# Kernel tuning notes

Measured on AMD Instinct MI355X. Metric: run time of the kernel, lower is better.

Reference implementation:

```python
import jax, jax.numpy as jnp
import numpy as np

D = 256; H = 8; FF = 1024; Q = 128; C = 512; B = 4
HD = D // H

def _ln(x, g, b):
    m = x.mean(-1, keepdims=True)
    v = ((x - m) ** 2).mean(-1, keepdims=True)
    return (x - m) / jnp.sqrt(v + 1e-5) * g + b

def _mha(q, k, v, in_w, in_b, out_w, out_b):
    # q,k,v: (L,B,D) / (S,B,D); in_w: (3D,D) packed q|k|v as in torch MHA
    qp = q @ in_w[:D].T + in_b[:D]
    kp = k @ in_w[D:2*D].T + in_b[D:2*D]
    vp = v @ in_w[2*D:].T + in_b[2*D:]
    L, Bb, _ = qp.shape; S = kp.shape[0]
    qh = qp.reshape(L, Bb, H, HD)
    kh = kp.reshape(S, Bb, H, HD)
    vh = vp.reshape(S, Bb, H, HD)
    scores = jnp.einsum('lbhd,sbhd->bhls', qh, kh) / np.sqrt(HD).astype(np.float32)
    a = jax.nn.softmax(scores, axis=-1)
    o = jnp.einsum('bhls,sbhd->lbhd', a, vh).reshape(L, Bb, D)
    return o @ out_w.T + out_b

def setup_inputs() -> dict:
    key = jax.random.key(0)
    ks = jax.random.split(key, 30)
    def p(k, shape, s=0.02):
        return jax.random.normal(k, shape, jnp.float32) * s
    return {
        'tgt': jax.random.normal(ks[0], (Q, B, D), jnp.float32),
        'memory': jax.random.normal(ks[1], (C, B, D), jnp.float32),
        'query_pos': jax.random.normal(ks[2], (Q, B, D), jnp.float32),
        'relative_pos': jax.random.normal(ks[3], (Q, C, B, D), jnp.float32),
        'ln1_g': jnp.ones((D,), jnp.float32), 'ln1_b': jnp.zeros((D,), jnp.float32),
        'ln2_g': jnp.ones((D,), jnp.float32), 'ln2_b': jnp.zeros((D,), jnp.float32),
        'ln3_g': jnp.ones((D,), jnp.float32), 'ln3_b': jnp.zeros((D,), jnp.float32),
        'in_proj_w': p(ks[4], (3 * D, D)), 'in_proj_b': jnp.zeros((3 * D,), jnp.float32),
        'attn_out_w': p(ks[5], (D, D)), 'attn_out_b': jnp.zeros((D,), jnp.float32),
        'mlp1_w': p(ks[6], (D, D)), 'mlp1_b': jnp.zeros((D,), jnp.float32),
        'mlp2_w': p(ks[7], (D, D)), 'mlp2_b': jnp.zeros((D,), jnp.float32),
        'v_w': p(ks[8], (D, D)), 'v_b': jnp.zeros((D,), jnp.float32),
        'o_w': p(ks[9], (D, D)), 'o_b': jnp.zeros((D,), jnp.float32),
        'ff1_w': p(ks[10], (FF, D)), 'ff1_b': jnp.zeros((FF,), jnp.float32),
        'ff2_w': p(ks[11], (D, FF)), 'ff2_b': jnp.zeros((D,), jnp.float32),
    }

def reference(tgt, memory, query_pos, relative_pos,
              ln1_g, ln1_b, ln2_g, ln2_b, ln3_g, ln3_b,
              in_proj_w, in_proj_b, attn_out_w, attn_out_b,
              mlp1_w, mlp1_b, mlp2_w, mlp2_b,
              v_w, v_b, o_w, o_b, ff1_w, ff1_b, ff2_w, ff2_b):
    # pre-norm self-attention (dropout = identity in eval)
    tgt2 = _ln(tgt, ln1_g, ln1_b)
    qk = tgt2 + query_pos
    sa = _mha(qk, qk, tgt2, in_proj_w, in_proj_b, attn_out_w, attn_out_b)
    tgt = tgt + sa
    # relation-attention branch
    tgt2 = _ln(tgt, ln2_g, ln2_b)                       # (Q,B,D)
    x = tgt2[:, None, :, :] - memory[None, :, :, :] + relative_pos  # (Q,C,B,D)
    h = jax.nn.relu(x @ mlp1_w.T + mlp1_b)
    sim = h @ mlp2_w.T + mlp2_b                          # (Q,C,B,D)
    attn = jax.nn.softmax(sim / np.sqrt(D).astype(np.float32), axis=1)
    v2 = (memory[None, :, :, :] + relative_pos) @ v_w.T + v_b
    t = jnp.einsum('qcbf,qcbf->qbf', attn, v2)           # (Q,B,D)
    t = jax.nn.relu(t @ o_w.T + o_b)
    tgt = t + tgt2
    # FFN
    tgt2 = _ln(tgt, ln3_g, ln3_b)
    ff = jax.nn.relu(tgt2 @ ff1_w.T + ff1_b) @ ff2_w.T + ff2_b
    return tgt + ff
```

## Files before the change

kernel.cpp:

```cpp
#include <hip/hip_runtime.h>
#include <hip/hip_bf16.h>
#include <cstdint>
#include <cstddef>

#define DEV __device__ __forceinline__

typedef __attribute__((ext_vector_type(8))) short short8;
typedef __attribute__((ext_vector_type(4))) float f32x4;

constexpr int Dm  = 256;
constexpr int Qn  = 128;
constexpr int Cn  = 512;
constexpr int Bn  = 4;

DEV unsigned short f2bf(float f){
  unsigned int u = __builtin_bit_cast(unsigned int, f);
  u += 0x7fffu + ((u >> 16) & 1u);
  return (unsigned short)(u >> 16);
}
DEV unsigned int pk2(float a, float b){
  return (unsigned int)f2bf(a) | ((unsigned int)f2bf(b) << 16);
}

DEV f32x4 mfma16(short8 a, short8 b, f32x4 c){
  return __builtin_amdgcn_mfma_f32_16x16x32_bf16(a, b, c, 0, 0, 0);
}

DEV short8 ldfrag(const unsigned short* buf, int rowbytes, int row0, int ks, int l){
  int r = row0 + (l & 15);
  int byte = (ks * 64 + ((l >> 4) * 16)) ^ ((r & 7) << 4);
  return *(const short8*)((const char*)buf + r * rowbytes + byte);
}

DEV void gload_lds16(const void* g, void* lds){
  __builtin_amdgcn_global_load_lds(
      (const __attribute__((address_space(1))) unsigned int*)g,
      (__attribute__((address_space(3))) unsigned int*)lds, 16, 0, 0);
}

DEV void packw(unsigned short* dst, const float* src, int j){
  int f = j >> 8, d = j & 255;
  int d8 = d >> 3, e = d & 7;
  int byte = (d8 * 16) ^ ((f & 15) << 4);
  dst[f * 256 + (byte >> 1) + e] = f2bf(src[j]);
}

__global__ __launch_bounds__(256) void conv_all_kernel(
    const float* inw, unsigned short* inw_bf,
    const float* aow, unsigned short* aow_bf,
    const float* ow,  unsigned short* ow_bf,
    const float* f1w, unsigned short* f1w_bf,
    const float* f2w, unsigned short* f2w_bf,
    const float* m1w, unsigned short* w1pk,
    const float* m2w, unsigned short* w2pk,
    const float* vw,  unsigned short* wvpk)
{
  const int total = 196608 + 65536 + 65536 + 262144 + 262144 + 3 * 65536;
  for (int i = blockIdx.x * 256 + threadIdx.x; i < total; i += gridDim.x * 256){
    int j = i;
    if (j < 196608){ inw_bf[j] = f2bf(inw[j]); continue; } j -= 196608;
    if (j < 65536) { aow_bf[j] = f2bf(aow[j]); continue; } j -= 65536;
    if (j < 65536) { ow_bf[j]  = f2bf(ow[j]);  continue; } j -= 65536;
    if (j < 262144){ f1w_bf[j] = f2bf(f1w[j]); continue; } j -= 262144;
    if (j < 262144){ f2w_bf[j] = f2bf(f2w[j]); continue; } j -= 262144;
    if (j < 65536) { packw(w1pk, m1w, j); continue; } j -= 65536;
    if (j < 65536) { packw(w2pk, m2w, j); continue; } j -= 65536;
    packw(wvpk, vw, j);
  }
}

__global__ __launch_bounds__(256) void ln_kernel(
    const float* __restrict__ in, const float* __restrict__ g, const float* __restrict__ bt,
    const float* __restrict__ addp,
    float* __restrict__ outF, unsigned short* __restrict__ outA, unsigned short* __restrict__ outB)
{
  const int r = blockIdx.x, t = threadIdx.x;
  float x = in[(size_t)r * 256 + t];
  float s = x, s2 = x * x;
  #pragma unroll
  for (int m = 1; m < 64; m <<= 1){ s += __shfl_xor(s, m, 64); s2 += __shfl_xor(s2, m, 64); }
  __shared__ float ls[8];
  int w = t >> 6, l = t & 63;
  if (l == 0){ ls[w] = s; ls[4 + w] = s2; }
  __syncthreads();
  s  = ls[0] + ls[1] + ls[2] + ls[3];
  s2 = ls[4] + ls[5] + ls[6] + ls[7];
  float mean = s * (1.f / 256.f);
  float var  = s2 * (1.f / 256.f) - mean * mean;
  float y = (x - mean) * rsqrtf(var + 1e-5f) * g[t] + bt[t];
  size_t o = (size_t)r * 256 + t;
  if (outF) outF[o] = y;
  if (outA) outA[o] = f2bf(y);
  if (outB) outB[o] = f2bf(y + addp[o]);
}

__global__ __launch_bounds__(256, 4) void gemm_kernel(
    const unsigned short* __restrict__ A, const unsigned short* __restrict__ W,
    const float* __restrict__ bias, const float* __restrict__ resid,
    float* __restrict__ Cf, unsigned short* __restrict__ Cb,
    int M, int N, int K, float alpha, int relu)
{
  __shared__ unsigned short As[64 * 64];
  __shared__ unsigned short Ws[64 * 64];
  const int tid = threadIdx.x;
  const int l = tid & 63;
  const int w = tid >> 6;
  const int wm = w >> 1, wn = w & 1;
  const int bm = blockIdx.x * 64, bn = blockIdx.y * 64;
  f32x4 acc[2][2] = {{{0,0,0,0},{0,0,0,0}},{{0,0,0,0},{0,0,0,0}}};

  for (int kc = 0; kc < K; kc += 64){
    __syncthreads();
    #pragma unroll
    for (int i = 0; i < 2; ++i){
      int idx = tid + i * 256;
      int r = idx >> 3, s = idx & 7;
      int byte = (s * 16) ^ ((r & 7) << 4);
      *(short8*)((char*)As + r * 128 + byte) = *(const short8*)(A + (size_t)(bm + r) * K + kc + s * 8);
      *(short8*)((char*)Ws + r * 128 + byte) = *(const short8*)(W + (size_t)(bn + r) * K + kc + s * 8);
    }
    __syncthreads();
    #pragma unroll
    for (int ks = 0; ks < 2; ++ks){
      short8 af[2], bf[2];
      af[0] = ldfrag(As, 128, wm * 32,      ks, l);
      af[1] = ldfrag(As, 128, wm * 32 + 16, ks, l);
      bf[0] = ldfrag(Ws, 128, wn * 32,      ks, l);
      bf[1] = ldfrag(Ws, 128, wn * 32 + 16, ks, l);
      #pragma unroll
      for (int i = 0; i < 2; ++i)
        #pragma unroll
        for (int j = 0; j < 2; ++j)
          acc[i][j] = mfma16(af[i], bf[j], acc[i][j]);
    }
  }
  #pragma unroll
  for (int i = 0; i < 2; ++i)
  #pragma unroll
  for (int j = 0; j < 2; ++j){
    int col = bn + wn * 32 + j * 16 + (l & 15);
    float bv = bias ? bias[col] : 0.f;
    #pragma unroll
    for (int u = 0; u < 4; ++u){
      int row = bm + wm * 32 + i * 16 + ((l >> 4) << 2) + u;
      float v = alpha * acc[i][j][u] + bv;
      if (relu) v = fmaxf(v, 0.f);
      if (resid) v += resid[(size_t)row * N + col];
      if (Cf) Cf[(size_t)row * N + col] = v;
      if (Cb) Cb[(size_t)row * N + col] = f2bf(v);
    }
  }
}

__global__ __launch_bounds__(256) void attn_kernel(
    const float* __restrict__ qkp, const float* __restrict__ vp,
    unsigned short* __restrict__ attn_o)
{
  __shared__ float ks[128][33];
  __shared__ float vs[128][33];
  __shared__ float sc[128][129];
  const int bh = blockIdx.x;
  const int b = bh >> 3, h = bh & 7;
  const int tid = threadIdx.x;
  const int lrow = tid >> 1;
  const int half = tid & 1;
  {
    int s = tid >> 1;
    int d0 = half * 16;
    const float* kp = qkp + ((size_t)s * Bn + b) * 512 + 256 + h * 32 + d0;
    const float* vv = vp  + ((size_t)s * Bn + b) * 256 +       h * 32 + d0;
    #pragma unroll
    for (int d = 0; d < 16; d += 4){
      *(float4*)&ks[s][d0 + d] = *(const float4*)(kp + d);
      *(float4*)&vs[s][d0 + d] = *(const float4*)(vv + d);
    }
  }
  __syncthreads();
  float qv[32];
  const float* qp = qkp + ((size_t)lrow * Bn + b) * 512 + h * 32;
  #pragma unroll
  for (int d = 0; d < 32; ++d) qv[d] = qp[d];
  const float scale = 0.17677669529663687f;
  float mloc = -1e30f;
  for (int s2 = 0; s2 < 64; ++s2){
    int s = half * 64 + s2;
    float dot = 0.f;
    #pragma unroll
    for (int d = 0; d < 32; ++d) dot += qv[d] * ks[s][d];
    dot *= scale;
    sc[lrow][s] = dot;
    mloc = fmaxf(mloc, dot);
  }
  float m = fmaxf(mloc, __shfl_xor(mloc, 1, 64));
  float sum = 0.f;
  for (int s2 = 0; s2 < 64; ++s2){
    int s = half * 64 + s2;
    float e = __expf(sc[lrow][s] - m);
    sum += e;
    sc[lrow][s] = e;
  }
  sum += __shfl_xor(sum, 1, 64);
  float inv = 1.f / sum;
  float o[32];
  #pragma unroll
  for (int d = 0; d < 32; ++d) o[d] = 0.f;
  for (int s2 = 0; s2 < 64; ++s2){
    int s = half * 64 + s2;
    float e = sc[lrow][s];
    #pragma unroll
    for (int d = 0; d < 32; ++d) o[d] += e * vs[s][d];
  }
  #pragma unroll
  for (int d = 0; d < 32; ++d){
    o[d] += __shfl_xor(o[d], 1, 64);
    o[d] *= inv;
  }
  unsigned short* op = attn_o + ((size_t)lrow * Bn + b) * 256 + h * 32 + half * 16;
  #pragma unroll
  for (int d = 0; d < 16; ++d) op[d] = f2bf(o[half * 16 + d]);
}

__global__ __launch_bounds__(512, 2) void relfused_kernel(
    const float* __restrict__ rel, const float* __restrict__ memp,
    const float* __restrict__ t22f,
    const unsigned short* __restrict__ W1g,
    const unsigned short* __restrict__ W2g,
    const unsigned short* __restrict__ Wvg,
    const float* __restrict__ b1, const float* __restrict__ b2,
    const float* __restrict__ vbp,
    unsigned short* __restrict__ trel)
{
  __shared__ unsigned short W1t[65536];
  __shared__ unsigned short xb[4096];
  __shared__ unsigned short yb[4096];
  __shared__ unsigned short hb[4096];

  const int qb = blockIdx.x;
  const int q = qb >> 2, b = qb & 3;
  const int tid = threadIdx.x;
  const int w = tid >> 6, l = tid & 63;
  const int l15 = l & 15, lg = l >> 4;

  #pragma unroll
  for (int i = 0; i < 16; ++i){
    int base = (w * 16 + i) * 64;
    gload_lds16((const char*)W1g + ((size_t)base + l) * 16, (char*)W1t + (size_t)base * 16);
  }

  short8 w2r[2][8], wvr[2][8];
  #pragma unroll
  for (int j = 0; j < 2; ++j){
    int f = w * 32 + j * 16 + l15;
    #pragma unroll
    for (int kc = 0; kc < 8; ++kc){
      int byte = f * 512 + ((kc * 64 + lg * 16) ^ ((f & 15) << 4));
      w2r[j][kc] = *(const short8*)((const char*)W2g + byte);
      wvr[j][kc] = *(const short8*)((const char*)Wvg + byte);
    }
  }

  float bv1[2][4], bv2[2][4], bvv[2][4];
  #pragma unroll
  for (int j = 0; j < 2; ++j)
    #pragma unroll
    for (int u = 0; u < 4; ++u){
      int f = w * 32 + j * 16 + lg * 4 + u;
      bv1[j][u] = b1[f]; bv2[j][u] = b2[f]; bvv[j][u] = vbp[f];
    }

  const int srow = tid >> 5, d8 = tid & 31;
  const int toff = srow * 512 + ((d8 * 16) ^ ((srow & 15) << 4));
  const float4 t20 = *(const float4*)(t22f + (size_t)qb * 256 + d8 * 8);
  const float4 t21 = *(const float4*)(t22f + (size_t)qb * 256 + d8 * 8 + 4);
  const float* relbase = rel + (((size_t)q * 512 + srow) * 4 + b) * 256 + d8 * 8;
  const float* membase = memp + ((size_t)(srow * 4 + b)) * 256 + d8 * 8;

  float4 r0 = *(const float4*)relbase;
  float4 r1 = *(const float4*)(relbase + 4);
  float4 m0 = *(const float4*)membase;
  float4 m1 = *(const float4*)(membase + 4);

  float ta[2][4], la[2][4];
  #pragma unroll
  for (int j = 0; j < 2; ++j)
    #pragma unroll
    for (int u = 0; u < 4; ++u){ ta[j][u] = 0.f; la[j][u] = 0.f; }

  for (int t = 0; t < 32; ++t){
    uint4 xw, yw;
    xw.x = pk2(t20.x - m0.x + r0.x, t20.y - m0.y + r0.y);
    xw.y = pk2(t20.z - m0.z + r0.z, t20.w - m0.w + r0.w);
    xw.z = pk2(t21.x - m1.x + r1.x, t21.y - m1.y + r1.y);
    xw.w = pk2(t21.z - m1.z + r1.z, t21.w - m1.w + r1.w);
    yw.x = pk2(r0.x + m0.x, r0.y + m0.y);
    yw.y = pk2(r0.z + m0.z, r0.w + m0.w);
    yw.z = pk2(r1.x + m1.x, r1.y + m1.y);
    yw.w = pk2(r1.z + m1.z, r1.w + m1.w);
    *(uint4*)((char*)xb + toff) = xw;
    *(uint4*)((char*)yb + toff) = yw;
    if (t < 31){
      const float* rp = relbase + (size_t)(t + 1) * 16384;
      const float* mp = membase + (size_t)(t + 1) * 16384;
      r0 = *(const float4*)rp;  r1 = *(const float4*)(rp + 4);
      m0 = *(const float4*)mp;  m1 = *(const float4*)(mp + 4);
    }
    if (t == 0) asm volatile("s_waitcnt vmcnt(0)" ::: "memory");
    __syncthreads();

    f32x4 acch[2] = {{0,0,0,0},{0,0,0,0}};
    #pragma unroll
    for (int kc = 0; kc < 8; ++kc){
      short8 bx = *(const short8*)((const char*)xb + l15 * 512 + ((kc * 64 + lg * 16) ^ (l15 << 4)));
      #pragma unroll
      for (int j = 0; j < 2; ++j){
        int f = w * 32 + j * 16 + l15;
        short8 aw = *(const short8*)((const char*)W1t + f * 512 + ((kc * 64 + lg * 16) ^ ((f & 15) << 4)));
        acch[j] = mfma16(aw, bx, acch[j]);
      }
    }
    #pragma unroll
    for (int j = 0; j < 2; ++j){
      uint2 hp;
      hp.x = pk2(fmaxf(acch[j][0] + bv1[j][0], 0.f), fmaxf(acch[j][1] + bv1[j][1], 0.f));
      hp.y = pk2(fmaxf(acch[j][2] + bv1[j][2], 0.f), fmaxf(acch[j][3] + bv1[j][3], 0.f));
      int inrow = (w * 64 + j * 32 + lg * 8) ^ (l15 << 4);
      *(uint2*)((char*)hb + l15 * 512 + inrow) = hp;
    }
    __syncthreads();

    f32x4 accs[2] = {{0,0,0,0},{0,0,0,0}};
    f32x4 accv[2] = {{0,0,0,0},{0,0,0,0}};
    #pragma unroll
    for (int kc = 0; kc < 8; ++kc){
      int inb = (kc * 64 + lg * 16) ^ (l15 << 4);
      short8 bh = *(const short8*)((const char*)hb + l15 * 512 + inb);
      short8 by = *(const short8*)((const char*)yb + l15 * 512 + inb);
      #pragma unroll
      for (int j = 0; j < 2; ++j){
        accs[j] = mfma16(w2r[j][kc], bh, accs[j]);
        accv[j] = mfma16(wvr[j][kc], by, accv[j]);
      }
    }
    #pragma unroll
    for (int j = 0; j < 2; ++j)
      #pragma unroll
      for (int u = 0; u < 4; ++u){
        float e = __expf((accs[j][u] + bv2[j][u]) * 0.0625f);
        float v2 = accv[j][u] + bvv[j][u];
        ta[j][u] += e * v2;
        la[j][u] += e;
      }
    if (t < 31) __syncthreads();
  }

  #pragma unroll
  for (int j = 0; j < 2; ++j)
    #pragma unroll
    for (int u = 0; u < 4; ++u){
      #pragma unroll
      for (int m = 1; m <= 8; m <<= 1){
        ta[j][u] += __shfl_xor(ta[j][u], m, 64);
        la[j][u] += __shfl_xor(la[j][u], m, 64);
      }
    }
  if (l15 == 0){
    #pragma unroll
    for (int j = 0; j < 2; ++j){
      uint2 o;
      o.x = pk2(ta[j][0] / la[j][0], ta[j][1] / la[j][1]);
      o.y = pk2(ta[j][2] / la[j][2], ta[j][3] / la[j][3]);
      *(uint2*)(trel + (size_t)qb * 256 + w * 32 + j * 16 + lg * 4) = o;
    }
  }
}

extern "C" void kernel_launch(void* const* d_in, const int* in_sizes, int n_in,
                              void* d_out, int out_size, void* d_ws, size_t ws_size,
                              hipStream_t stream)
{
  const float* tgt  = (const float*)d_in[0];
  const float* mem  = (const float*)d_in[1];
  const float* qpos = (const float*)d_in[2];
  const float* rel  = (const float*)d_in[3];
  const float* ln1g = (const float*)d_in[4];
  const float* ln1b = (const float*)d_in[5];
  const float* ln2g = (const float*)d_in[6];
  const float* ln2b = (const float*)d_in[7];
  const float* ln3g = (const float*)d_in[8];
  const float* ln3b = (const float*)d_in[9];
  const float* inw  = (const float*)d_in[10];
  const float* inb  = (const float*)d_in[11];
  const float* aow  = (const float*)d_in[12];
  const float* aob  = (const float*)d_in[13];
  const float* m1w  = (const float*)d_in[14];
  const float* m1b  = (const float*)d_in[15];
  const float* m2w  = (const float*)d_in[16];
  const float* m2b  = (const float*)d_in[17];
  const float* vw   = (const float*)d_in[18];
  const float* vb   = (const float*)d_in[19];
  const float* ow   = (const float*)d_in[20];
  const float* ob   = (const float*)d_in[21];
  const float* f1w  = (const float*)d_in[22];
  const float* f1b  = (const float*)d_in[23];
  const float* f2w  = (const float*)d_in[24];
  const float* f2b  = (const float*)d_in[25];

  char* ws = (char*)d_ws;
  size_t off = 0;
  auto alloc = [&](size_t bytes) -> char* {
    char* p = ws + off; off += (bytes + 255) & ~size_t(255); return p;
  };
  unsigned short* w1pk    = (unsigned short*)alloc(256 * 256 * 2);
  unsigned short* w2pk    = (unsigned short*)alloc(256 * 256 * 2);
  unsigned short* wvpk    = (unsigned short*)alloc(256 * 256 * 2);
  unsigned short* inw_bf  = (unsigned short*)alloc(768 * 256 * 2);
  unsigned short* aow_bf  = (unsigned short*)alloc(256 * 256 * 2);
  unsigned short* ow_bf   = (unsigned short*)alloc(256 * 256 * 2);
  unsigned short* f1w_bf  = (unsigned short*)alloc(1024 * 256 * 2);
  unsigned short* f2w_bf  = (unsigned short*)alloc(256 * 1024 * 2);
  unsigned short* t21_bf  = (unsigned short*)alloc(512 * 256 * 2);
  unsigned short* qk_bf   = (unsigned short*)alloc(512 * 256 * 2);
  float*          qkp     = (float*)alloc(512 * 512 * 4);
  float*          vp      = (float*)alloc(512 * 256 * 4);
  unsigned short* ao_bf   = (unsigned short*)alloc(512 * 256 * 2);
  float*          tgta    = (float*)alloc(512 * 256 * 4);
  float*          t22_f   = (float*)alloc(512 * 256 * 4);
  unsigned short* trel_bf = (unsigned short*)alloc(512 * 256 * 2);
  float*          tgtr    = (float*)alloc(512 * 256 * 4);
  unsigned short* t23_bf  = (unsigned short*)alloc(512 * 256 * 2);
  unsigned short* ffh_bf  = (unsigned short*)alloc(512 * 1024 * 2);

  conv_all_kernel<<<2048, 256, 0, stream>>>(inw, inw_bf, aow, aow_bf, ow, ow_bf,
      f1w, f1w_bf, f2w, f2w_bf, m1w, w1pk, m2w, w2pk, vw, wvpk);

  ln_kernel<<<512, 256, 0, stream>>>(tgt, ln1g, ln1b, qpos, nullptr, t21_bf, qk_bf);

  gemm_kernel<<<dim3(8, 8), 256, 0, stream>>>(qk_bf, inw_bf, inb, nullptr,
      qkp, nullptr, 512, 512, 256, 1.f, 0);
  gemm_kernel<<<dim3(8, 4), 256, 0, stream>>>(t21_bf, inw_bf + 512 * 256, inb + 512, nullptr,
      vp, nullptr, 512, 256, 256, 1.f, 0);

  attn_kernel<<<32, 256, 0, stream>>>(qkp, vp, ao_bf);

  gemm_kernel<<<dim3(8, 4), 256, 0, stream>>>(ao_bf, aow_bf, aob, tgt,
      tgta, nullptr, 512, 256, 256, 1.f, 0);

  ln_kernel<<<512, 256, 0, stream>>>(tgta, ln2g, ln2b, nullptr, t22_f, nullptr, nullptr);

  relfused_kernel<<<512, 512, 0, stream>>>(rel, mem, t22_f, w1pk, w2pk, wvpk,
      m1b, m2b, vb, trel_bf);

  gemm_kernel<<<dim3(8, 4), 256, 0, stream>>>(trel_bf, ow_bf, ob, t22_f,
      tgtr, nullptr, 512, 256, 256, 1.f, 1);

  ln_kernel<<<512, 256, 0, stream>>>(tgtr, ln3g, ln3b, nullptr, nullptr, t23_bf, nullptr);

  gemm_kernel<<<dim3(8, 16), 256, 0, stream>>>(t23_bf, f1w_bf, f1b, nullptr,
      nullptr, ffh_bf, 512, 1024, 256, 1.f, 1);
  gemm_kernel<<<dim3(8, 4), 256, 0, stream>>>(ffh_bf, f2w_bf, f2b, tgtr,
      (float*)d_out, nullptr, 512, 256, 1024, 1.f, 0);
}
```

Baseline: 331.0 us.

## Keep W1 in registers, double-buffer relation tiles, fold biases out of loop

The relation kernel now holds W1 in registers instead of a 128KB LDS copy, and double-buffers the x/y/h tiles so the second GEMM stage of step t-1 overlaps with the first stage of step t. The mlp2 bias is dropped, since a per-feature constant cancels in a softmax over C. The v bias is added once after normalisation instead of on every element. This cuts LDS footprint and synchronisation per step, but about 192 registers of weights per thread under launch_bounds(512,2) risks register spilling.

```diff
diff --git a/kernel.cpp b/kernel.cpp
--- a/kernel.cpp
+++ b/kernel.cpp
@@ -30,12 +30,6 @@
   int r = row0 + (l & 15);
   int byte = (ks * 64 + ((l >> 4) * 16)) ^ ((r & 7) << 4);
   return *(const short8*)((const char*)buf + r * rowbytes + byte);
-}
-
-DEV void gload_lds16(const void* g, void* lds){
-  __builtin_amdgcn_global_load_lds(
-      (const __attribute__((address_space(1))) unsigned int*)g,
-      (__attribute__((address_space(3))) unsigned int*)lds, 16, 0, 0);
 }
 
 DEV void packw(unsigned short* dst, const float* src, int j){
@@ -226,14 +220,15 @@
     const unsigned short* __restrict__ W1g,
     const unsigned short* __restrict__ W2g,
     const unsigned short* __restrict__ Wvg,
-    const float* __restrict__ b1, const float* __restrict__ b2,
+    const float* __restrict__ b1,
     const float* __restrict__ vbp,
     unsigned short* __restrict__ trel)
 {
-  __shared__ unsigned short W1t[65536];
-  __shared__ unsigned short xb[4096];
-  __shared__ unsigned short yb[4096];
-  __shared__ unsigned short hb[4096];
+  __shared__ unsigned short xb[2][4096];
+  __shared__ unsigned short yb[2][4096];
+  __shared__ unsigned short hb[2][4096];
+  __shared__ float t2s[256];
+  __shared__ float b1s[256];
 
   const int qb = blockIdx.x;
   const int q = qb >> 2, b = qb & 3;
@@ -241,53 +236,36 @@
   const int w = tid >> 6, l = tid & 63;
   const int l15 = l & 15, lg = l >> 4;
 
-  #pragma unroll
-  for (int i = 0; i < 16; ++i){
-    int base = (w * 16 + i) * 64;
-    gload_lds16((const char*)W1g + ((size_t)base + l) * 16, (char*)W1t + (size_t)base * 16);
-  }
-
-  short8 w2r[2][8], wvr[2][8];
+  if (tid < 256){ t2s[tid] = t22f[(size_t)qb * 256 + tid]; b1s[tid] = b1[tid]; }
+
+  short8 w1r[2][8], w2r[2][8], wvr[2][8];
   #pragma unroll
   for (int j = 0; j < 2; ++j){
     int f = w * 32 + j * 16 + l15;
     #pragma unroll
     for (int kc = 0; kc < 8; ++kc){
       int byte = f * 512 + ((kc * 64 + lg * 16) ^ ((f & 15) << 4));
+      w1r[j][kc] = *(const short8*)((const char*)W1g + byte);
       w2r[j][kc] = *(const short8*)((const char*)W2g + byte);
       wvr[j][kc] = *(const short8*)((const char*)Wvg + byte);
     }
   }
 
-  float bv1[2][4], bv2[2][4], bvv[2][4];
-  #pragma unroll
-  for (int j = 0; j < 2; ++j)
-    #pragma unroll
-    for (int u = 0; u < 4; ++u){
-      int f = w * 32 + j * 16 + lg * 4 + u;
-      bv1[j][u] = b1[f]; bv2[j][u] = b2[f]; bvv[j][u] = vbp[f];
-    }
-
   const int srow = tid >> 5, d8 = tid & 31;
   const int toff = srow * 512 + ((d8 * 16) ^ ((srow & 15) << 4));
-  const float4 t20 = *(const float4*)(t22f + (size_t)qb * 256 + d8 * 8);
-  const float4 t21 = *(const float4*)(t22f + (size_t)qb * 256 + d8 * 8 + 4);
   const float* relbase = rel + (((size_t)q * 512 + srow) * 4 + b) * 256 + d8 * 8;
   const float* membase = memp + ((size_t)(srow * 4 + b)) * 256 + d8 * 8;
 
-  float4 r0 = *(const float4*)relbase;
-  float4 r1 = *(const float4*)(relbase + 4);
-  float4 m0 = *(const float4*)membase;
-  float4 m1 = *(const float4*)(membase + 4);
-
   float ta[2][4], la[2][4];
   #pragma unroll
   for (int j = 0; j < 2; ++j)
     #pragma unroll
     for (int u = 0; u < 4; ++u){ ta[j][u] = 0.f; la[j][u] = 0.f; }
 
-  for (int t = 0; t < 32; ++t){
-    uint4 xw, yw;
+  uint4 xw, yw;
+  auto packxy = [&](const float4& r0, const float4& r1, const float4& m0, const float4& m1){
+    float4 t20 = *(const float4*)&t2s[d8 * 8];
+    float4 t21 = *(const float4*)&t2s[d8 * 8 + 4];
     xw.x = pk2(t20.x - m0.x + r0.x, t20.y - m0.y + r0.y);
     xw.y = pk2(t20.z - m0.z + r0.z, t20.w - m0.w + r0.w);
     xw.z = pk2(t21.x - m1.x + r1.x, t21.y - m1.y + r1.y);
@@ -296,45 +274,18 @@
     yw.y = pk2(r0.z + m0.z, r0.w + m0.w);
     yw.z = pk2(r1.x + m1.x, r1.y + m1.y);
     yw.w = pk2(r1.z + m1.z, r1.w + m1.w);
-    *(uint4*)((char*)xb + toff) = xw;
-    *(uint4*)((char*)yb + toff) = yw;
-    if (t < 31){
-      const float* rp = relbase + (size_t)(t + 1) * 16384;
-      const float* mp = membase + (size_t)(t + 1) * 16384;
-      r0 = *(const float4*)rp;  r1 = *(const float4*)(rp + 4);
-      m0 = *(const float4*)mp;  m1 = *(const float4*)(mp + 4);
-    }
-    if (t == 0) asm volatile("s_waitcnt vmcnt(0)" ::: "memory");
-    __syncthreads();
-
-    f32x4 acch[2] = {{0,0,0,0},{0,0,0,0}};
-    #pragma unroll
-    for (int kc = 0; kc < 8; ++kc){
-      short8 bx = *(const short8*)((const char*)xb + l15 * 512 + ((kc * 64 + lg * 16) ^ (l15 << 4)));
-      #pragma unroll
-      for (int j = 0; j < 2; ++j){
-        int f = w * 32 + j * 16 + l15;
-        short8 aw = *(const short8*)((const char*)W1t + f * 512 + ((kc * 64 + lg * 16) ^ ((f & 15) << 4)));
-        acch[j] = mfma16(aw, bx, acch[j]);
-      }
-    }
-    #pragma unroll
-    for (int j = 0; j < 2; ++j){
-      uint2 hp;
-      hp.x = pk2(fmaxf(acch[j][0] + bv1[j][0], 0.f), fmaxf(acch[j][1] + bv1[j][1], 0.f));
-      hp.y = pk2(fmaxf(acch[j][2] + bv1[j][2], 0.f), fmaxf(acch[j][3] + bv1[j][3], 0.f));
-      int inrow = (w * 64 + j * 32 + lg * 8) ^ (l15 << 4);
-      *(uint2*)((char*)hb + l15 * 512 + inrow) = hp;
-    }
-    __syncthreads();
-
+  };
+
+  auto phase2 = [&](int pb){
+    const char* hbp = (const char*)hb + pb * 8192;
+    const char* ybp = (const char*)yb + pb * 8192;
     f32x4 accs[2] = {{0,0,0,0},{0,0,0,0}};
     f32x4 accv[2] = {{0,0,0,0},{0,0,0,0}};
     #pragma unroll
     for (int kc = 0; kc < 8; ++kc){
-      int inb = (kc * 64 + lg * 16) ^ (l15 << 4);
-      short8 bh = *(const short8*)((const char*)hb + l15 * 512 + inb);
-      short8 by = *(const short8*)((const char*)yb + l15 * 512 + inb);
+      int inb = l15 * 512 + ((kc * 64 + lg * 16) ^ (l15 << 4));
+      short8 bh = *(const short8*)(hbp + inb);
+      short8 by = *(const short8*)(ybp + inb);
       #pragma unroll
       for (int j = 0; j < 2; ++j){
         accs[j] = mfma16(w2r[j][kc], bh, accs[j]);
@@ -345,13 +296,67 @@
     for (int j = 0; j < 2; ++j)
       #pragma unroll
       for (int u = 0; u < 4; ++u){
-        float e = __expf((accs[j][u] + bv2[j][u]) * 0.0625f);
-        float v2 = accv[j][u] + bvv[j][u];
-        ta[j][u] += e * v2;
+        float e = __expf(accs[j][u] * 0.0625f);
+        ta[j][u] += e * accv[j][u];
         la[j][u] += e;
       }
-    if (t < 31) __syncthreads();
-  }
+  };
+
+  float4 r0 = *(const float4*)relbase;
+  float4 r1 = *(const float4*)(relbase + 4);
+  float4 m0 = *(const float4*)membase;
+  float4 m1 = *(const float4*)(membase + 4);
+  __syncthreads();
+  packxy(r0, r1, m0, m1);
+  *(uint4*)((char*)xb + toff) = xw;
+  *(uint4*)((char*)yb + toff) = yw;
+  r0 = *(const float4*)(relbase + 16384);
+  r1 = *(const float4*)(relbase + 16384 + 4);
+  m0 = *(const float4*)(membase + 16384);
+  m1 = *(const float4*)(membase + 16384 + 4);
+
+  for (int t = 0; t < 32; ++t){
+    __syncthreads();
+    const char* xbp = (const char*)xb + (t & 1) * 8192;
+    f32x4 acch[2] = {{0,0,0,0},{0,0,0,0}};
+    #pragma unroll
+    for (int kc = 0; kc < 8; ++kc){
+      short8 bx = *(const short8*)(xbp + l15 * 512 + ((kc * 64 + lg * 16) ^ (l15 << 4)));
+      #pragma unroll
+      for (int j = 0; j < 2; ++j)
+        acch[j] = mfma16(w1r[j][kc], bx, acch[j]);
+    }
+    {
+      char* hbp = (char*)hb + (t & 1) * 8192;
+      #pragma unroll
+      for (int j = 0; j < 2; ++j){
+        float4 bb = *(const float4*)&b1s[w * 32 + j * 16 + lg * 4];
+        uint2 hp;
+        hp.x = pk2(fmaxf(acch[j][0] + bb.x, 0.f), fmaxf(acch[j][1] + bb.y, 0.f));
+        hp.y = pk2(fmaxf(acch[j][2] + bb.z, 0.f), fmaxf(acch[j][3] + bb.w, 0.f));
+        int inrow = (w * 64 + j * 32 + lg * 8) ^ (l15 << 4);
+        *(uint2*)(hbp + l15 * 512 + inrow) = hp;
+      }
+    }
+    if (t < 31) packxy(r0, r1, m0, m1);
+    if (t > 0) phase2((t - 1) & 1);
+    if (t < 31){
+      __syncthreads();
+      char* xbn = (char*)xb + ((t + 1) & 1) * 8192;
+      char* ybn = (char*)yb + ((t + 1) & 1) * 8192;
+      *(uint4*)(xbn + toff) = xw;
+      *(uint4*)(ybn + toff) = yw;
+      if (t < 30){
+        size_t o = (size_t)(t + 2) * 16384;
+        r0 = *(const float4*)(relbase + o);
+        r1 = *(const float4*)(relbase + o + 4);
+        m0 = *(const float4*)(membase + o);
+        m1 = *(const float4*)(membase + o + 4);
+      }
+    }
+  }
+  __syncthreads();
+  phase2(1);
 
   #pragma unroll
   for (int j = 0; j < 2; ++j)
@@ -366,9 +371,10 @@
   if (l15 == 0){
     #pragma unroll
     for (int j = 0; j < 2; ++j){
+      float4 vb4 = *(const float4*)(vbp + w * 32 + j * 16 + lg * 4);
       uint2 o;
-      o.x = pk2(ta[j][0] / la[j][0], ta[j][1] / la[j][1]);
-      o.y = pk2(ta[j][2] / la[j][2], ta[j][3] / la[j][3]);
+      o.x = pk2(ta[j][0] / la[j][0] + vb4.x, ta[j][1] / la[j][1] + vb4.y);
+      o.y = pk2(ta[j][2] / la[j][2] + vb4.z, ta[j][3] / la[j][3] + vb4.w);
       *(uint2*)(trel + (size_t)qb * 256 + w * 32 + j * 16 + lg * 4) = o;
     }
   }
@@ -448,7 +454,7 @@
   ln_kernel<<<512, 256, 0, stream>>>(tgta, ln2g, ln2b, nullptr, t22_f, nullptr, nullptr);
 
   relfused_kernel<<<512, 512, 0, stream>>>(rel, mem, t22_f, w1pk, w2pk, wvpk,
-      m1b, m2b, vb, trel_bf);
+      m1b, vb, trel_bf);
 
   gemm_kernel<<<dim3(8, 4), 256, 0, stream>>>(trel_bf, ow_bf, ob, t22_f,
       tgtr, nullptr, 512, 256, 256, 1.f, 1);
```

New measurement: 373.3 us. 1.13x slower.

## Restructure relation kernel with async double-buffered LDS loads and register weights

Applied to the files above, without the earlier changes.

The relation-attention kernel moves to 1024 threads per block. Each wave now keeps its 16-feature slice of all three weight matrices (W1, W2, Wv) in registers, so W1 no longer has to be staged in LDS. Tiles of relative_pos and a bf16 copy of memory are streamed into double-buffered LDS with global_load_lds, processing 32 context rows per step so the next tile's load overlaps compute. The mlp2 bias is dropped because it is constant along the softmax axis, and the value bias is added after normalisation. Memory is converted to bf16 once in the setup kernel, which adds extra work there and a small rounding change to memory.

```diff
diff --git a/kernel.cpp b/kernel.cpp
--- a/kernel.cpp
+++ b/kernel.cpp
@@ -18,6 +18,8 @@
   u += 0x7fffu + ((u >> 16) & 1u);
   return (unsigned short)(u >> 16);
 }
+DEV float bfl(unsigned int u){ return __builtin_bit_cast(float, u << 16); }
+DEV float bfh(unsigned int u){ return __builtin_bit_cast(float, u & 0xffff0000u); }
 DEV unsigned int pk2(float a, float b){
   return (unsigned int)f2bf(a) | ((unsigned int)f2bf(b) << 16);
 }
@@ -53,9 +55,10 @@
     const float* f2w, unsigned short* f2w_bf,
     const float* m1w, unsigned short* w1pk,
     const float* m2w, unsigned short* w2pk,
-    const float* vw,  unsigned short* wvpk)
-{
-  const int total = 196608 + 65536 + 65536 + 262144 + 262144 + 3 * 65536;
+    const float* vw,  unsigned short* wvpk,
+    const float* memp, unsigned short* mem_bf)
+{
+  const int total = 196608 + 65536 + 65536 + 262144 + 262144 + 3 * 65536 + 524288;
   for (int i = blockIdx.x * 256 + threadIdx.x; i < total; i += gridDim.x * 256){
     int j = i;
     if (j < 196608){ inw_bf[j] = f2bf(inw[j]); continue; } j -= 196608;
@@ -65,7 +68,8 @@
     if (j < 262144){ f2w_bf[j] = f2bf(f2w[j]); continue; } j -= 262144;
     if (j < 65536) { packw(w1pk, m1w, j); continue; } j -= 65536;
     if (j < 65536) { packw(w2pk, m2w, j); continue; } j -= 65536;
-    packw(wvpk, vw, j);
+    if (j < 65536) { packw(wvpk, vw, j);  continue; } j -= 65536;
+    mem_bf[j] = f2bf(memp[j]);
   }
 }
 
@@ -220,20 +224,23 @@
   for (int d = 0; d < 16; ++d) op[d] = f2bf(o[half * 16 + d]);
 }
 
-__global__ __launch_bounds__(512, 2) void relfused_kernel(
-    const float* __restrict__ rel, const float* __restrict__ memp,
+__global__ __launch_bounds__(1024) void relfused_kernel(
+    const float* __restrict__ rel, const unsigned short* __restrict__ mem_bf,
     const float* __restrict__ t22f,
     const unsigned short* __restrict__ W1g,
     const unsigned short* __restrict__ W2g,
     const unsigned short* __restrict__ Wvg,
-    const float* __restrict__ b1, const float* __restrict__ b2,
+    const float* __restrict__ b1,
     const float* __restrict__ vbp,
     unsigned short* __restrict__ trel)
 {
-  __shared__ unsigned short W1t[65536];
-  __shared__ unsigned short xb[4096];
-  __shared__ unsigned short yb[4096];
-  __shared__ unsigned short hb[4096];
+  __shared__ char relbuf[2 * 32768];
+  __shared__ char membuf[2 * 16384];
+  __shared__ char xb[16384];
+  __shared__ char yb[16384];
+  __shared__ char hb[16384];
+  __shared__ float t2s[256];
+  __shared__ float b1s[256];
 
   const int qb = blockIdx.x;
   const int q = qb >> 2, b = qb & 3;
@@ -241,136 +248,134 @@
   const int w = tid >> 6, l = tid & 63;
   const int l15 = l & 15, lg = l >> 4;
 
-  #pragma unroll
-  for (int i = 0; i < 16; ++i){
-    int base = (w * 16 + i) * 64;
-    gload_lds16((const char*)W1g + ((size_t)base + l) * 16, (char*)W1t + (size_t)base * 16);
-  }
-
-  short8 w2r[2][8], wvr[2][8];
-  #pragma unroll
-  for (int j = 0; j < 2; ++j){
-    int f = w * 32 + j * 16 + l15;
+  if (tid < 256){ t2s[tid] = t22f[(size_t)qb * 256 + tid]; b1s[tid] = b1[tid]; }
+
+  short8 w1r[8], w2r[8], wvr[8];
+  {
+    const size_t F = (size_t)(w * 16 + l15);
     #pragma unroll
     for (int kc = 0; kc < 8; ++kc){
-      int byte = f * 512 + ((kc * 64 + lg * 16) ^ ((f & 15) << 4));
-      w2r[j][kc] = *(const short8*)((const char*)W2g + byte);
-      wvr[j][kc] = *(const short8*)((const char*)Wvg + byte);
-    }
-  }
-
-  float bv1[2][4], bv2[2][4], bvv[2][4];
-  #pragma unroll
-  for (int j = 0; j < 2; ++j)
-    #pragma unroll
-    for (int u = 0; u < 4; ++u){
-      int f = w * 32 + j * 16 + lg * 4 + u;
-      bv1[j][u] = b1[f]; bv2[j][u] = b2[f]; bvv[j][u] = vbp[f];
-    }
-
-  const int srow = tid >> 5, d8 = tid & 31;
-  const int toff = srow * 512 + ((d8 * 16) ^ ((srow & 15) << 4));
-  const float4 t20 = *(const float4*)(t22f + (size_t)qb * 256 + d8 * 8);
-  const float4 t21 = *(const float4*)(t22f + (size_t)qb * 256 + d8 * 8 + 4);
-  const float* relbase = rel + (((size_t)q * 512 + srow) * 4 + b) * 256 + d8 * 8;
-  const float* membase = memp + ((size_t)(srow * 4 + b)) * 256 + d8 * 8;
-
-  float4 r0 = *(const float4*)relbase;
-  float4 r1 = *(const float4*)(relbase + 4);
-  float4 m0 = *(const float4*)membase;
-  float4 m1 = *(const float4*)(membase + 4);
-
-  float ta[2][4], la[2][4];
-  #pragma unroll
-  for (int j = 0; j < 2; ++j)
-    #pragma unroll
-    for (int u = 0; u < 4; ++u){ ta[j][u] = 0.f; la[j][u] = 0.f; }
-
-  for (int t = 0; t < 32; ++t){
-    uint4 xw, yw;
-    xw.x = pk2(t20.x - m0.x + r0.x, t20.y - m0.y + r0.y);
-    xw.y = pk2(t20.z - m0.z + r0.z, t20.w - m0.w + r0.w);
-    xw.z = pk2(t21.x - m1.x + r1.x, t21.y - m1.y + r1.y);
-    xw.w = pk2(t21.z - m1.z + r1.z, t21.w - m1.w + r1.w);
-    yw.x = pk2(r0.x + m0.x, r0.y + m0.y);
-    yw.y = pk2(r0.z + m0.z, r0.w + m0.w);
-    yw.z = pk2(r1.x + m1.x, r1.y + m1.y);
-    yw.w = pk2(r1.z + m1.z, r1.w + m1.w);
-    *(uint4*)((char*)xb + toff) = xw;
-    *(uint4*)((char*)yb + toff) = yw;
-    if (t < 31){
-      const float* rp = relbase + (size_t)(t + 1) * 16384;
-      const float* mp = membase + (size_t)(t + 1) * 16384;
-      r0 = *(const float4*)rp;  r1 = *(const float4*)(rp + 4);
-      m0 = *(const float4*)mp;  m1 = *(const float4*)(mp + 4);
-    }
-    if (t == 0) asm volatile("s_waitcnt vmcnt(0)" ::: "memory");
+      size_t byte = F * 512 + (size_t)((kc * 64 + lg * 16) ^ (l15 << 4));
+      w1r[kc] = *(const short8*)((const char*)W1g + byte);
+      w2r[kc] = *(const short8*)((const char*)W2g + byte);
+      wvr[kc] = *(const short8*)((const char*)Wvg + byte);
+    }
+  }
+
+  auto issue = [&](int tp){
+    const int p = tp & 1;
+    const int c0 = tp * 32;
+    #pragma unroll
+    for (int i = 0; i < 2; ++i){
+      int c = c0 + 2 * w + i;
+      gload_lds16(rel + (((size_t)q * 512 + c) * 4 + b) * 256 + l * 4,
+                  relbuf + p * 32768 + (2 * w + i) * 1024);
+    }
+    int c = c0 + 2 * w + (l >> 5);
+    gload_lds16(mem_bf + ((size_t)(c * 4 + b)) * 256 + (l & 31) * 8,
+                membuf + p * 16384 + w * 1024);
+  };
+
+  float ta[4] = {0.f, 0.f, 0.f, 0.f}, la[4] = {0.f, 0.f, 0.f, 0.f};
+
+  issue(0);
+
+  for (int t = 0; t < 16; ++t){
+    if (t < 15){
+      issue(t + 1);
+      asm volatile("s_waitcnt vmcnt(3)" ::: "memory");
+    } else {
+      asm volatile("s_waitcnt vmcnt(0)" ::: "memory");
+    }
+    __builtin_amdgcn_sched_barrier(0);
     __syncthreads();
 
-    f32x4 acch[2] = {{0,0,0,0},{0,0,0,0}};
-    #pragma unroll
-    for (int kc = 0; kc < 8; ++kc){
-      short8 bx = *(const short8*)((const char*)xb + l15 * 512 + ((kc * 64 + lg * 16) ^ (l15 << 4)));
+    {
+      const int cr = tid >> 5, d8 = tid & 31;
+      const char* rbp = relbuf + (t & 1) * 32768 + cr * 1024;
+      const char* mbp = membuf + (t & 1) * 16384 + cr * 512;
+      int swz = (cr & 15) << 4;
+      int bo1 = cr * 512 + ((((d8 >> 1) * 16) ^ swz) | ((d8 & 1) * 8));
+      int bo2 = cr * 512 + ((((16 + (d8 >> 1)) * 16) ^ swz) | ((d8 & 1) * 8));
+      {
+        float4 ra = *(const float4*)(rbp + d8 * 16);
+        uint2  ma = *(const uint2*)(mbp + d8 * 8);
+        float4 t4 = *(const float4*)((const char*)t2s + d8 * 16);
+        float m0 = bfl(ma.x), m1 = bfh(ma.x), m2 = bfl(ma.y), m3 = bfh(ma.y);
+        uint2 xw, yw;
+        xw.x = pk2(t4.x - m0 + ra.x, t4.y - m1 + ra.y);
+        xw.y = pk2(t4.z - m2 + ra.z, t4.w - m3 + ra.w);
+        yw.x = pk2(ra.x + m0, ra.y + m1);
+        yw.y = pk2(ra.z + m2, ra.w + m3);
+        *(uint2*)(xb + bo1) = xw;
+        *(uint2*)(yb + bo1) = yw;
+      }
+      {
+        float4 ra = *(const float4*)(rbp + 512 + d8 * 16);
+        uint2  ma = *(const uint2*)(mbp + 256 + d8 * 8);
+        float4 t4 = *(const float4*)((const char*)t2s + 512 + d8 * 16);
+        float m0 = bfl(ma.x), m1 = bfh(ma.x), m2 = bfl(ma.y), m3 = bfh(ma.y);
+        uint2 xw, yw;
+        xw.x = pk2(t4.x - m0 + ra.x, t4.y - m1 + ra.y);
+        xw.y = pk2(t4.z - m2 + ra.z, t4.w - m3 + ra.w);
+        yw.x = pk2(ra.x + m0, ra.y + m1);
+        yw.y = pk2(ra.z + m2, ra.w + m3);
+        *(uint2*)(xb + bo2) = xw;
+        *(uint2*)(yb + bo2) = yw;
+      }
+    }
+    __syncthreads();
+
+    #pragma unroll
+    for (int cs = 0; cs < 2; ++cs){
+      f32x4 acc = {0.f, 0.f, 0.f, 0.f};
+      const char* xrow = xb + (cs * 16 + l15) * 512;
       #pragma unroll
-      for (int j = 0; j < 2; ++j){
-        int f = w * 32 + j * 16 + l15;
-        short8 aw = *(const short8*)((const char*)W1t + f * 512 + ((kc * 64 + lg * 16) ^ ((f & 15) << 4)));
-        acch[j] = mfma16(aw, bx, acch[j]);
+      for (int kc = 0; kc < 8; ++kc)
+        acc = mfma16(w1r[kc], *(const short8*)(xrow + ((kc * 64 + lg * 16) ^ (l15 << 4))), acc);
+      float4 bb = *(const float4*)&b1s[w * 16 + lg * 4];
+      uint2 hp;
+      hp.x = pk2(fmaxf(acc[0] + bb.x, 0.f), fmaxf(acc[1] + bb.y, 0.f));
+      hp.y = pk2(fmaxf(acc[2] + bb.z, 0.f), fmaxf(acc[3] + bb.w, 0.f));
+      int ro = w * 32 + lg * 8;
+      *(uint2*)(hb + (cs * 16 + l15) * 512 + (((ro & ~15) ^ (l15 << 4)) | (ro & 8))) = hp;
+    }
+    __syncthreads();
+
+    #pragma unroll
+    for (int cs = 0; cs < 2; ++cs){
+      f32x4 as = {0.f, 0.f, 0.f, 0.f}, av = {0.f, 0.f, 0.f, 0.f};
+      const char* hrow = hb + (cs * 16 + l15) * 512;
+      const char* yrow = yb + (cs * 16 + l15) * 512;
+      #pragma unroll
+      for (int kc = 0; kc < 8; ++kc){
+        int off = (kc * 64 + lg * 16) ^ (l15 << 4);
+        as = mfma16(w2r[kc], *(const short8*)(hrow + off), as);
+        av = mfma16(wvr[kc], *(const short8*)(yrow + off), av);
       }
-    }
-    #pragma unroll
-    for (int j = 0; j < 2; ++j){
-      uint2 hp;
-      hp.x = pk2(fmaxf(acch[j][0] + bv1[j][0], 0.f), fmaxf(acch[j][1] + bv1[j][1], 0.f));
-      hp.y = pk2(fmaxf(acch[j][2] + bv1[j][2], 0.f), fmaxf(acch[j][3] + bv1[j][3], 0.f));
-      int inrow = (w * 64 + j * 32 + lg * 8) ^ (l15 << 4);
-      *(uint2*)((char*)hb + l15 * 512 + inrow) = hp;
-    }
-    __syncthreads();
-
-    f32x4 accs[2] = {{0,0,0,0},{0,0,0,0}};
-    f32x4 accv[2] = {{0,0,0,0},{0,0,0,0}};
-    #pragma unroll
-    for (int kc = 0; kc < 8; ++kc){
-      int inb = (kc * 64 + lg * 16) ^ (l15 << 4);
-      short8 bh = *(const short8*)((const char*)hb + l15 * 512 + inb);
-      short8 by = *(const short8*)((const char*)yb + l15 * 512 + inb);
-      #pragma unroll
-      for (int j = 0; j < 2; ++j){
-        accs[j] = mfma16(w2r[j][kc], bh, accs[j]);
-        accv[j] = mfma16(wvr[j][kc], by, accv[j]);
-      }
-    }
-    #pragma unroll
-    for (int j = 0; j < 2; ++j)
       #pragma unroll
       for (int u = 0; u < 4; ++u){
-        float e = __expf((accs[j][u] + bv2[j][u]) * 0.0625f);
-        float v2 = accv[j][u] + bvv[j][u];
-        ta[j][u] += e * v2;
-        la[j][u] += e;
+        float e = __expf(as[u] * 0.0625f);
+        ta[u] += e * av[u];
+        la[u] += e;
       }
-    if (t < 31) __syncthreads();
-  }
-
-  #pragma unroll
-  for (int j = 0; j < 2; ++j)
-    #pragma unroll
-    for (int u = 0; u < 4; ++u){
-      #pragma unroll
-      for (int m = 1; m <= 8; m <<= 1){
-        ta[j][u] += __shfl_xor(ta[j][u], m, 64);
-        la[j][u] += __shfl_xor(la[j][u], m, 64);
-      }
-    }
+    }
+  }
+
+  #pragma unroll
+  for (int u = 0; u < 4; ++u){
+    #pragma unroll
+    for (int m = 1; m <= 8; m <<= 1){
+      ta[u] += __shfl_xor(ta[u], m, 64);
+      la[u] += __shfl_xor(la[u], m, 64);
+    }
+  }
   if (l15 == 0){
-    #pragma unroll
-    for (int j = 0; j < 2; ++j){
-      uint2 o;
-      o.x = pk2(ta[j][0] / la[j][0], ta[j][1] / la[j][1]);
-      o.y = pk2(ta[j][2] / la[j][2], ta[j][3] / la[j][3]);
-      *(uint2*)(trel + (size_t)qb * 256 + w * 32 + j * 16 + lg * 4) = o;
-    }
+    float4 vb4 = *(const float4*)(vbp + w * 16 + lg * 4);
+    uint2 o;
+    o.x = pk2(ta[0] / la[0] + vb4.x, ta[1] / la[1] + vb4.y);
+    o.y = pk2(ta[2] / la[2] + vb4.z, ta[3] / la[3] + vb4.w);
+    *(uint2*)(trel + (size_t)qb * 256 + w * 16 + lg * 4) = o;
   }
 }
 
@@ -413,6 +418,7 @@
   unsigned short* w1pk    = (unsigned short*)alloc(256 * 256 * 2);
   unsigned short* w2pk    = (unsigned short*)alloc(256 * 256 * 2);
   unsigned short* wvpk    = (unsigned short*)alloc(256 * 256 * 2);
+  unsigned short* mem_bf  = (unsigned short*)alloc(2048 * 256 * 2);
   unsigned short* inw_bf  = (unsigned short*)alloc(768 * 256 * 2);
   unsigned short* aow_bf  = (unsigned short*)alloc(256 * 256 * 2);
   unsigned short* ow_bf   = (unsigned short*)alloc(256 * 256 * 2);
@@ -431,7 +437,7 @@
   unsigned short* ffh_bf  = (unsigned short*)alloc(512 * 1024 * 2);
 
   conv_all_kernel<<<2048, 256, 0, stream>>>(inw, inw_bf, aow, aow_bf, ow, ow_bf,
-      f1w, f1w_bf, f2w, f2w_bf, m1w, w1pk, m2w, w2pk, vw, wvpk);
+      f1w, f1w_bf, f2w, f2w_bf, m1w, w1pk, m2w, w2pk, vw, wvpk, mem, mem_bf);
 
   ln_kernel<<<512, 256, 0, stream>>>(tgt, ln1g, ln1b, qpos, nullptr, t21_bf, qk_bf);
 
@@ -447,8 +453,8 @@
 
   ln_kernel<<<512, 256, 0, stream>>>(tgta, ln2g, ln2b, nullptr, t22_f, nullptr, nullptr);
 
-  relfused_kernel<<<512, 512, 0, stream>>>(rel, mem, t22_f, w1pk, w2pk, wvpk,
-      m1b, m2b, vb, trel_bf);
+  relfused_kernel<<<512, 1024, 0, stream>>>(rel, mem_bf, t22_f, w1pk, w2pk, wvpk,
+      m1b, vb, trel_bf);
 
   gemm_kernel<<<dim3(8, 4), 256, 0, stream>>>(trel_bf, ow_bf, ob, t22_f,
       tgtr, nullptr, 512, 256, 256, 1.f, 1);
```

New measurement: 607.9 us. 1.84x slower.
